# Kernel optimization log

Measured on AMD Instinct MI355X. Metric: run time of the kernel, lower is better.

## Reference

```python
import jax, jax.numpy as jnp
import numpy as np

N_NODES = 50000
N_EDGES = 800000
IN_CH, HID_CH, OUT_CH = 128, 128, 64


def setup_inputs() -> dict:
    key = jax.random.key(0)
    k1, k2, k3, k4 = jax.random.split(key, 4)
    x = jax.random.normal(k1, (N_NODES, IN_CH), dtype=jnp.float32)
    edge_index = jax.random.randint(k2, (2, N_EDGES), 0, N_NODES, dtype=jnp.int64)
    # Glorot-style scaled weights (as in PyG GCNConv default init)
    W1 = jax.random.normal(k3, (IN_CH, HID_CH), dtype=jnp.float32) * (1.0 / np.sqrt(IN_CH))
    b1 = jnp.zeros((HID_CH,), dtype=jnp.float32)
    W2 = jax.random.normal(k4, (HID_CH, OUT_CH), dtype=jnp.float32) * (1.0 / np.sqrt(HID_CH))
    b2 = jnp.zeros((OUT_CH,), dtype=jnp.float32)
    return {"x": x, "edge_index": edge_index, "W1": W1, "b1": b1, "W2": W2, "b2": b2}


def _gcn_conv(x, src, dst, norm, W, b, n_nodes):
    # linear transform, then normalized gather-scatter aggregation
    h = x @ W                                   # [N, C_out]
    msgs = h[src] * norm[:, None]               # [E+N, C_out]
    agg = jax.ops.segment_sum(msgs, dst, num_segments=n_nodes)
    return agg + b


def reference(x, edge_index, W1, b1, W2, b2):
    n = x.shape[0]
    # add self-loops (PyG GCNConv default)
    loops = jnp.arange(n, dtype=edge_index.dtype)
    src = jnp.concatenate([edge_index[0], loops])  # message source (x_j)
    dst = jnp.concatenate([edge_index[1], loops])  # aggregation target
    # symmetric normalization: deg computed over targets incl. self-loops
    deg = jax.ops.segment_sum(jnp.ones_like(dst, dtype=x.dtype), dst, num_segments=n)
    dinv = jnp.where(deg > 0, jax.lax.rsqrt(deg), 0.0)
    norm = dinv[src] * dinv[dst]                # [E+N]

    h = _gcn_conv(x, src, dst, norm, W1, b1, n)
    h = jax.nn.relu(h)
    out = _gcn_conv(h, src, dst, norm, W2, b2, n)
    return out
```

## Files before the change

kernel.cpp:

```cpp
#include <hip/hip_runtime.h>
#include <hip/hip_bf16.h>


#define NPB 196
#define NBMAX 1024
#define CAP 4096

__device__ __forceinline__ unsigned short f2bf(float f) {
    unsigned int u = __float_as_uint(f);
    unsigned int r = u + 0x7fffu + ((u >> 16) & 1u);
    return (unsigned short)(r >> 16);
}

__global__ void k_zerob(int* __restrict__ p, int n) {
    int i = blockIdx.x * blockDim.x + threadIdx.x;
    if (i < n) p[i] = 0;
}

__global__ __launch_bounds__(256) void k_bhist(const int* __restrict__ dst,
                                               int* __restrict__ bhist,
                                               int nb, int e) {
    __shared__ int hist[NBMAX];
    const int tid = threadIdx.x;
    for (int b = tid; b < nb; b += 256) hist[b] = 0;
    __syncthreads();
    for (int i = blockIdx.x * 256 + tid; i < e; i += gridDim.x * 256)
        atomicAdd(&hist[dst[i] / NPB], 1);
    __syncthreads();
    for (int b = tid; b < nb; b += 256)
        if (hist[b]) atomicAdd(&bhist[b], hist[b]);
}

__global__ __launch_bounds__(64) void k_bscan(const int* __restrict__ bhist,
                                              int* __restrict__ bbase,
                                              int* __restrict__ bcursor,
                                              int nb, int e) {
    const int lane = threadIdx.x;
    int carry = 0;
    for (int base = 0; base < nb; base += 64) {
        int i = base + lane;
        int v = (i < nb) ? bhist[i] : 0;
        int s = v;
#pragma unroll
        for (int d = 1; d < 64; d <<= 1) {
            int u = __shfl_up(s, d);
            if (lane >= d) s += u;
        }
        int excl = carry + s - v;
        if (i < nb) { bbase[i] = excl; bcursor[i] = excl; }
        carry += __shfl(s, 63);
    }
    if (lane == 0) bbase[nb] = e;
}

__global__ __launch_bounds__(256) void k_bpart(const int* __restrict__ src,
                                               const int* __restrict__ dst,
                                               int* __restrict__ bcursor,
                                               int2* __restrict__ part,
                                               int nb, int e, int cpb) {
    __shared__ int chist[NBMAX];
    __shared__ int cbase[NBMAX];
    const int tid = threadIdx.x;
    const int e0 = blockIdx.x * cpb;
    const int e1 = min(e, e0 + cpb);
    for (int b = tid; b < nb; b += 256) chist[b] = 0;
    __syncthreads();
    for (int i = e0 + tid; i < e1; i += 256)
        atomicAdd(&chist[dst[i] / NPB], 1);
    __syncthreads();
    for (int b = tid; b < nb; b += 256) {
        int c = chist[b];
        cbase[b] = c ? atomicAdd(&bcursor[b], c) : 0;
        chist[b] = 0;
    }
    __syncthreads();
    for (int i = e0 + tid; i < e1; i += 256) {
        int d = dst[i];
        int bkt = d / NPB;
        int l = atomicAdd(&chist[bkt], 1);
        part[cbase[bkt] + l] = make_int2(src[i], d);
    }
}

__global__ __launch_bounds__(256) void k_bcsr(const int2* __restrict__ part,
                                              const int* __restrict__ bbase,
                                              int* __restrict__ offs,
                                              float* __restrict__ dinv,
                                              int* __restrict__ srcs,
                                              int n, int e) {
    __shared__ int cntL[256];
    __shared__ int srcsL[CAP];
    const int b = blockIdx.x;
    const int tid = threadIdx.x;
    const int eb0 = bbase[b], eb1 = bbase[b + 1];
    const int cnt = eb1 - eb0;
    const int n0 = b * NPB;
    const int npb = min(NPB, n - n0);

    if (tid < 256) cntL[tid] = 0;
    __syncthreads();
    for (int i = eb0 + tid; i < eb1; i += 256)
        atomicAdd(&cntL[part[i].y - n0], 1);
    __syncthreads();

    if (tid < 64) {
        const int lane = tid;
        int carry = 0;
        for (int base = 0; base < npb; base += 64) {
            int i = base + lane;
            int v = (i < npb) ? cntL[i] : 0;
            int s = v;
#pragma unroll
            for (int d = 1; d < 64; d <<= 1) {
                int u = __shfl_up(s, d);
                if (lane >= d) s += u;
            }
            int excl = carry + s - v;
            if (i < npb) {
                offs[n0 + i] = eb0 + excl;
                dinv[n0 + i] = rsqrtf((float)(v + 1));
                cntL[i] = excl;
            }
            carry += __shfl(s, 63);
        }
    }
    if (b == gridDim.x - 1 && tid == 0) offs[n] = e;
    __syncthreads();

    if (cnt <= CAP) {
        for (int i = eb0 + tid; i < eb1; i += 256) {
            int2 pr = part[i];
            int pos = atomicAdd(&cntL[pr.y - n0], 1);
            srcsL[pos] = pr.x;
        }
        __syncthreads();
        for (int i = tid; i < cnt; i += 256)
            srcs[eb0 + i] = srcsL[i];
    } else {
        for (int i = eb0 + tid; i < eb1; i += 256) {
            int2 pr = part[i];
            int pos = atomicAdd(&cntL[pr.y - n0], 1);
            srcs[eb0 + pos] = pr.x;
        }
    }
}

template <int BN, bool RELU_A>
__global__ __launch_bounds__(256) void k_gemm(const float* __restrict__ A,
                                              const float* __restrict__ W,
                                              const float* __restrict__ dinv,
                                              unsigned short* __restrict__ Cout,
                                              int M, int Ntot) {
    __shared__ float As[64][132];
    __shared__ float Bs[128][BN];

    const int tid = threadIdx.x;
    const int bm = blockIdx.x * 64;
    const int bn = blockIdx.y * BN;

    constexpr int WF4 = 128 * BN / 4;
    for (int idx = tid; idx < WF4; idx += 256) {
        int row = idx / (BN / 4);
        int c4 = idx % (BN / 4);
        float4 v = *(const float4*)&W[row * Ntot + bn + c4 * 4];
        *(float4*)&Bs[row][c4 * 4] = v;
    }
    for (int idx = tid; idx < 64 * 32; idx += 256) {
        int row = idx >> 5;
        int c4 = idx & 31;
        int gr = bm + row;
        float4 v = make_float4(0.f, 0.f, 0.f, 0.f);
        if (gr < M) v = *(const float4*)&A[gr * 128 + c4 * 4];
        if (RELU_A) {
            v.x = fmaxf(v.x, 0.f); v.y = fmaxf(v.y, 0.f);
            v.z = fmaxf(v.z, 0.f); v.w = fmaxf(v.w, 0.f);
        }
        *(float4*)&As[row][c4 * 4] = v;
    }
    __syncthreads();

    const int ty = tid >> 4;
    const int tx = tid & 15;
    float acc[4][4] = {};

    for (int k = 0; k < 128; k += 4) {
        float av[4][4], bv[4][4];
#pragma unroll
        for (int i = 0; i < 4; ++i) {
            float4 t = *(const float4*)&As[ty * 4 + i][k];
            av[i][0] = t.x; av[i][1] = t.y; av[i][2] = t.z; av[i][3] = t.w;
        }
#pragma unroll
        for (int kk = 0; kk < 4; ++kk) {
            float4 t = *(const float4*)&Bs[k + kk][tx * 4];
            bv[kk][0] = t.x; bv[kk][1] = t.y; bv[kk][2] = t.z; bv[kk][3] = t.w;
        }
#pragma unroll
        for (int i = 0; i < 4; ++i)
#pragma unroll
            for (int kk = 0; kk < 4; ++kk)
#pragma unroll
                for (int j = 0; j < 4; ++j)
                    acc[i][j] = fmaf(av[i][kk], bv[kk][j], acc[i][j]);
    }

#pragma unroll
    for (int i = 0; i < 4; ++i) {
        int gr = bm + ty * 4 + i;
        if (gr < M) {
            float s = dinv[gr];
            ushort4 o;
            o.x = f2bf(acc[i][0] * s); o.y = f2bf(acc[i][1] * s);
            o.z = f2bf(acc[i][2] * s); o.w = f2bf(acc[i][3] * s);
            *(ushort4*)&Cout[(size_t)gr * Ntot + bn + tx * 4] = o;
        }
    }
}

template <int C>
__global__ __launch_bounds__(256) void k_aggr(const unsigned short* __restrict__ hs,
                                              const int* __restrict__ srcs,
                                              const int* __restrict__ offs,
                                              const float* __restrict__ dinv,
                                              const float* __restrict__ bias,
                                              float* __restrict__ outp, int n) {
    constexpr int ROWB = C * 2;
    constexpr int LPE  = ROWB / 16;
    constexpr int EPL  = 64 / LPE;
    constexpr int CHUNK = 16;
    __shared__ __align__(1024) char smem[4][CHUNK * ROWB];

    const int lane = threadIdx.x & 63;
    const int wid  = threadIdx.x >> 6;
    const int node = blockIdx.x * 4 + wid;
    if (node >= n) return;
    char* region = smem[wid];

    float2 acc = make_float2(0.f, 0.f);

    const int off = offs[node], end = offs[node + 1];
    for (int base = off; base < end; base += 64) {
        const int m = end - base;
        int p = 0;
        if (lane < m) p = srcs[base + lane];
        const int cnt = m < 64 ? m : 64;

        for (int j0 = 0; j0 < cnt; j0 += CHUNK) {
            const int cc = min(CHUNK, cnt - j0);
            const int nload = (cc + EPL - 1) / EPL;
            for (int l = 0; l < nload; ++l) {
                int e = j0 + l * EPL + (lane / LPE);
                int srow = __shfl(p, e);
                const char* ga = (const char*)hs + (size_t)srow * ROWB + (lane % LPE) * 16;
                __builtin_amdgcn_global_load_lds(
                    (const __attribute__((address_space(1))) unsigned int*)ga,
                    (__attribute__((address_space(3))) unsigned int*)(region + l * 1024),
                    16, 0, 0);
            }
            asm volatile("s_waitcnt vmcnt(0)" ::: "memory");
            __builtin_amdgcn_sched_barrier(0);

            if (C == 128) {
                for (int j = 0; j < cc; ++j) {
                    unsigned int u = *(const unsigned int*)(region + j * ROWB + lane * 4);
                    acc.x += __uint_as_float(u << 16);
                    acc.y += __uint_as_float(u & 0xffff0000u);
                }
            } else {
                const int half = lane >> 5;
                const int rounds = (cc + 1) >> 1;
                for (int r = 0; r < rounds; ++r) {
                    int e = r * 2 + half;
                    unsigned int u = *(const unsigned int*)(region + e * ROWB + (lane & 31) * 4);
                    if (e >= cc) u = 0u;
                    acc.x += __uint_as_float(u << 16);
                    acc.y += __uint_as_float(u & 0xffff0000u);
                }
            }
        }
    }

    if (C == 128) {
        unsigned int u = *(const unsigned int*)((const char*)hs + (size_t)node * ROWB + lane * 4);
        acc.x += __uint_as_float(u << 16);
        acc.y += __uint_as_float(u & 0xffff0000u);
        float di = dinv[node];
        float2 bb = *(const float2*)&bias[lane * 2];
        acc.x = fmaf(acc.x, di, bb.x);
        acc.y = fmaf(acc.y, di, bb.y);
        *(float2*)&outp[(size_t)node * C + lane * 2] = acc;
    } else {
        acc.x += __shfl_xor(acc.x, 32);
        acc.y += __shfl_xor(acc.y, 32);
        if (lane < 32) {
            unsigned int u = *(const unsigned int*)((const char*)hs + (size_t)node * ROWB + lane * 4);
            acc.x += __uint_as_float(u << 16);
            acc.y += __uint_as_float(u & 0xffff0000u);
            float di = dinv[node];
            float2 bb = *(const float2*)&bias[lane * 2];
            acc.x = fmaf(acc.x, di, bb.x);
            acc.y = fmaf(acc.y, di, bb.y);
            *(float2*)&outp[(size_t)node * C + lane * 2] = acc;
        }
    }
}

extern "C" void kernel_launch(void* const* d_in, const int* in_sizes, int n_in,
                              void* d_out, int out_size, void* d_ws, size_t ws_size,
                              hipStream_t stream) {
    const float* x  = (const float*)d_in[0];
    const int*   ei = (const int*)d_in[1];
    const float* W1 = (const float*)d_in[2];
    const float* b1 = (const float*)d_in[3];
    const float* W2 = (const float*)d_in[4];
    const float* b2 = (const float*)d_in[5];
    float* out = (float*)d_out;

    const int N = in_sizes[0] / 128;
    const int E = in_sizes[1] / 2;
    const int* src = ei;
    const int* dst = ei + E;
    const int NB = (N + NPB - 1) / NPB;
    const int CPB = (E + 255) / 256;

    char* wsb = (char*)d_ws;
    size_t o = 0;
    auto alloc = [&](size_t bytes, size_t align) {
        o = (o + align - 1) & ~(align - 1);
        char* p = wsb + o;
        o += bytes;
        return p;
    };
    int*   bhist  = (int*)alloc((size_t)NB * 4, 4);
    int*   bbase  = (int*)alloc((size_t)(NB + 1) * 4, 4);
    int*   bcur   = (int*)alloc((size_t)NB * 4, 4);
    int2*  part   = (int2*)alloc((size_t)E * 8, 8);
    int*   offs   = (int*)alloc((size_t)(N + 1) * 4, 4);
    float* dinv   = (float*)alloc((size_t)N * 4, 4);
    int*   srcs   = (int*)alloc((size_t)E * 4, 4);
    unsigned short* hs1 = (unsigned short*)alloc((size_t)N * 128 * 2, 16);
    unsigned short* hs2 = (unsigned short*)alloc((size_t)N * 64 * 2, 16);
    float* agg1   = (float*)alloc((size_t)N * 128 * 4, 16);

    k_zerob<<<1, 1024, 0, stream>>>(bhist, NB);
    k_bhist<<<256, 256, 0, stream>>>(dst, bhist, NB, E);
    k_bscan<<<1, 64, 0, stream>>>(bhist, bbase, bcur, NB, E);
    k_bpart<<<256, 256, 0, stream>>>(src, dst, bcur, part, NB, E, CPB);
    k_bcsr<<<NB, 256, 0, stream>>>(part, bbase, offs, dinv, srcs, N, E);

    const int gm = (N + 63) / 64;
    const int ga = (N + 3) / 4;

    k_gemm<64, false><<<dim3(gm, 2), 256, 0, stream>>>(x, W1, dinv, hs1, N, 128);
    k_aggr<128><<<ga, 256, 0, stream>>>(hs1, srcs, offs, dinv, b1, agg1, N);

    k_gemm<64, true><<<dim3(gm, 1), 256, 0, stream>>>(agg1, W2, dinv, hs2, N, 64);
    k_aggr<64><<<ga, 256, 0, stream>>>(hs2, srcs, offs, dinv, b2, out, N);
}
```

Baseline: 168.5 us.

## Use bf16 MFMA for GEMMs and store layer-1 output as relu'd bf16

```diff
diff --git a/kernel.cpp b/kernel.cpp
--- a/kernel.cpp
+++ b/kernel.cpp
@@ -5,6 +5,9 @@
 #define NPB 196
 #define NBMAX 1024
 #define CAP 4096
+
+using short8 = __attribute__((ext_vector_type(8))) short;
+using f32x4  = __attribute__((ext_vector_type(4))) float;
 
 __device__ __forceinline__ unsigned short f2bf(float f) {
     unsigned int u = __float_as_uint(f);
@@ -145,85 +148,105 @@
     }
 }
 
-template <int BN, bool RELU_A>
-__global__ __launch_bounds__(256) void k_gemm(const float* __restrict__ A,
+template <bool SRC_BF16>
+__global__ __launch_bounds__(256) void k_gemm(const void* __restrict__ A,
                                               const float* __restrict__ W,
                                               const float* __restrict__ dinv,
                                               unsigned short* __restrict__ Cout,
                                               int M, int Ntot) {
-    __shared__ float As[64][132];
-    __shared__ float Bs[128][BN];
+    __shared__ __align__(16) unsigned short As_b[64][136];
+    __shared__ __align__(16) unsigned short Bs_b[64][136];
 
     const int tid = threadIdx.x;
     const int bm = blockIdx.x * 64;
-    const int bn = blockIdx.y * BN;
-
-    constexpr int WF4 = 128 * BN / 4;
-    for (int idx = tid; idx < WF4; idx += 256) {
-        int row = idx / (BN / 4);
-        int c4 = idx % (BN / 4);
-        float4 v = *(const float4*)&W[row * Ntot + bn + c4 * 4];
-        *(float4*)&Bs[row][c4 * 4] = v;
-    }
-    for (int idx = tid; idx < 64 * 32; idx += 256) {
+    const int bn = blockIdx.y * 64;
+
+#pragma unroll
+    for (int t = 0; t < 8; ++t) {
+        int idx = tid + t * 256;
         int row = idx >> 5;
         int c4 = idx & 31;
         int gr = bm + row;
-        float4 v = make_float4(0.f, 0.f, 0.f, 0.f);
-        if (gr < M) v = *(const float4*)&A[gr * 128 + c4 * 4];
-        if (RELU_A) {
-            v.x = fmaxf(v.x, 0.f); v.y = fmaxf(v.y, 0.f);
-            v.z = fmaxf(v.z, 0.f); v.w = fmaxf(v.w, 0.f);
-        }
-        *(float4*)&As[row][c4 * 4] = v;
-    }
-    __syncthreads();
-
-    const int ty = tid >> 4;
-    const int tx = tid & 15;
-    float acc[4][4] = {};
-
-    for (int k = 0; k < 128; k += 4) {
-        float av[4][4], bv[4][4];
-#pragma unroll
-        for (int i = 0; i < 4; ++i) {
-            float4 t = *(const float4*)&As[ty * 4 + i][k];
-            av[i][0] = t.x; av[i][1] = t.y; av[i][2] = t.z; av[i][3] = t.w;
-        }
-#pragma unroll
-        for (int kk = 0; kk < 4; ++kk) {
-            float4 t = *(const float4*)&Bs[k + kk][tx * 4];
-            bv[kk][0] = t.x; bv[kk][1] = t.y; bv[kk][2] = t.z; bv[kk][3] = t.w;
-        }
-#pragma unroll
-        for (int i = 0; i < 4; ++i)
-#pragma unroll
-            for (int kk = 0; kk < 4; ++kk)
-#pragma unroll
-                for (int j = 0; j < 4; ++j)
-                    acc[i][j] = fmaf(av[i][kk], bv[kk][j], acc[i][j]);
-    }
-
-#pragma unroll
-    for (int i = 0; i < 4; ++i) {
-        int gr = bm + ty * 4 + i;
-        if (gr < M) {
-            float s = dinv[gr];
-            ushort4 o;
-            o.x = f2bf(acc[i][0] * s); o.y = f2bf(acc[i][1] * s);
-            o.z = f2bf(acc[i][2] * s); o.w = f2bf(acc[i][3] * s);
-            *(ushort4*)&Cout[(size_t)gr * Ntot + bn + tx * 4] = o;
-        }
-    }
-}
-
-template <int C>
+        ushort4 o = make_ushort4(0, 0, 0, 0);
+        if (SRC_BF16) {
+            if (gr < M)
+                o = *(const ushort4*)&((const unsigned short*)A)[(size_t)gr * 128 + c4 * 4];
+        } else {
+            if (gr < M) {
+                float4 f = *(const float4*)&((const float*)A)[(size_t)gr * 128 + c4 * 4];
+                o = make_ushort4(f2bf(f.x), f2bf(f.y), f2bf(f.z), f2bf(f.w));
+            }
+        }
+        *(ushort4*)&As_b[row][c4 * 4] = o;
+    }
+
+#pragma unroll
+    for (int t = 0; t < 2; ++t) {
+        int idx = tid + t * 256;
+        int kb = idx >> 4;
+        int c4 = idx & 15;
+        int k0 = kb * 4;
+        float4 f0 = *(const float4*)&W[(size_t)(k0 + 0) * Ntot + bn + c4 * 4];
+        float4 f1 = *(const float4*)&W[(size_t)(k0 + 1) * Ntot + bn + c4 * 4];
+        float4 f2 = *(const float4*)&W[(size_t)(k0 + 2) * Ntot + bn + c4 * 4];
+        float4 f3 = *(const float4*)&W[(size_t)(k0 + 3) * Ntot + bn + c4 * 4];
+        *(ushort4*)&Bs_b[c4 * 4 + 0][k0] =
+            make_ushort4(f2bf(f0.x), f2bf(f1.x), f2bf(f2.x), f2bf(f3.x));
+        *(ushort4*)&Bs_b[c4 * 4 + 1][k0] =
+            make_ushort4(f2bf(f0.y), f2bf(f1.y), f2bf(f2.y), f2bf(f3.y));
+        *(ushort4*)&Bs_b[c4 * 4 + 2][k0] =
+            make_ushort4(f2bf(f0.z), f2bf(f1.z), f2bf(f2.z), f2bf(f3.z));
+        *(ushort4*)&Bs_b[c4 * 4 + 3][k0] =
+            make_ushort4(f2bf(f0.w), f2bf(f1.w), f2bf(f2.w), f2bf(f3.w));
+    }
+    __syncthreads();
+
+    const int w = tid >> 6;
+    const int l = tid & 63;
+    const int wr = (w >> 1) * 32;
+    const int wc = (w & 1) * 32;
+    const int fr = l & 15;
+    const int fk = (l >> 4) * 8;
+
+    f32x4 acc[2][2] = {};
+
+#pragma unroll
+    for (int ks = 0; ks < 4; ++ks) {
+        const int kof = ks * 32 + fk;
+        short8 a0 = *(const short8*)&As_b[wr + fr][kof];
+        short8 a1 = *(const short8*)&As_b[wr + 16 + fr][kof];
+        short8 b0 = *(const short8*)&Bs_b[wc + fr][kof];
+        short8 b1 = *(const short8*)&Bs_b[wc + 16 + fr][kof];
+        acc[0][0] = __builtin_amdgcn_mfma_f32_16x16x32_bf16(a0, b0, acc[0][0], 0, 0, 0);
+        acc[0][1] = __builtin_amdgcn_mfma_f32_16x16x32_bf16(a0, b1, acc[0][1], 0, 0, 0);
+        acc[1][0] = __builtin_amdgcn_mfma_f32_16x16x32_bf16(a1, b0, acc[1][0], 0, 0, 0);
+        acc[1][1] = __builtin_amdgcn_mfma_f32_16x16x32_bf16(a1, b1, acc[1][1], 0, 0, 0);
+    }
+
+#pragma unroll
+    for (int i = 0; i < 2; ++i) {
+#pragma unroll
+        for (int r = 0; r < 4; ++r) {
+            int gr = bm + wr + i * 16 + ((l >> 4) << 2) + r;
+            if (gr < M) {
+                float s = dinv[gr];
+#pragma unroll
+                for (int j = 0; j < 2; ++j) {
+                    int gc = bn + wc + j * 16 + (l & 15);
+                    Cout[(size_t)gr * Ntot + gc] = f2bf(acc[i][j][r] * s);
+                }
+            }
+        }
+    }
+}
+
+template <int C, bool OBF>
 __global__ __launch_bounds__(256) void k_aggr(const unsigned short* __restrict__ hs,
                                               const int* __restrict__ srcs,
                                               const int* __restrict__ offs,
                                               const float* __restrict__ dinv,
                                               const float* __restrict__ bias,
-                                              float* __restrict__ outp, int n) {
+                                              void* __restrict__ outp, int n) {
     constexpr int ROWB = C * 2;
     constexpr int LPE  = ROWB / 16;
     constexpr int EPL  = 64 / LPE;
@@ -280,27 +303,25 @@
         }
     }
 
-    if (C == 128) {
+    if (C == 64) {
+        acc.x += __shfl_xor(acc.x, 32);
+        acc.y += __shfl_xor(acc.y, 32);
+        if (lane >= 32) return;
+    }
+    {
         unsigned int u = *(const unsigned int*)((const char*)hs + (size_t)node * ROWB + lane * 4);
         acc.x += __uint_as_float(u << 16);
         acc.y += __uint_as_float(u & 0xffff0000u);
         float di = dinv[node];
         float2 bb = *(const float2*)&bias[lane * 2];
-        acc.x = fmaf(acc.x, di, bb.x);
-        acc.y = fmaf(acc.y, di, bb.y);
-        *(float2*)&outp[(size_t)node * C + lane * 2] = acc;
-    } else {
-        acc.x += __shfl_xor(acc.x, 32);
-        acc.y += __shfl_xor(acc.y, 32);
-        if (lane < 32) {
-            unsigned int u = *(const unsigned int*)((const char*)hs + (size_t)node * ROWB + lane * 4);
-            acc.x += __uint_as_float(u << 16);
-            acc.y += __uint_as_float(u & 0xffff0000u);
-            float di = dinv[node];
-            float2 bb = *(const float2*)&bias[lane * 2];
-            acc.x = fmaf(acc.x, di, bb.x);
-            acc.y = fmaf(acc.y, di, bb.y);
-            *(float2*)&outp[(size_t)node * C + lane * 2] = acc;
+        float vx = fmaf(acc.x, di, bb.x);
+        float vy = fmaf(acc.y, di, bb.y);
+        if (OBF) {
+            unsigned short* ob = (unsigned short*)outp;
+            ushort2 o = make_ushort2(f2bf(fmaxf(vx, 0.f)), f2bf(fmaxf(vy, 0.f)));
+            *(ushort2*)&ob[(size_t)node * C + lane * 2] = o;
+        } else {
+            *(float2*)&((float*)outp)[(size_t)node * C + lane * 2] = make_float2(vx, vy);
         }
     }
 }
@@ -338,9 +359,9 @@
     int*   offs   = (int*)alloc((size_t)(N + 1) * 4, 4);
     float* dinv   = (float*)alloc((size_t)N * 4, 4);
     int*   srcs   = (int*)alloc((size_t)E * 4, 4);
-    unsigned short* hs1 = (unsigned short*)alloc((size_t)N * 128 * 2, 16);
-    unsigned short* hs2 = (unsigned short*)alloc((size_t)N * 64 * 2, 16);
-    float* agg1   = (float*)alloc((size_t)N * 128 * 4, 16);
+    unsigned short* hs1   = (unsigned short*)alloc((size_t)N * 128 * 2, 16);
+    unsigned short* hs2   = (unsigned short*)alloc((size_t)N * 64 * 2, 16);
+    unsigned short* agg1b = (unsigned short*)alloc((size_t)N * 128 * 2, 16);
 
     k_zerob<<<1, 1024, 0, stream>>>(bhist, NB);
     k_bhist<<<256, 256, 0, stream>>>(dst, bhist, NB, E);
@@ -351,9 +372,9 @@
     const int gm = (N + 63) / 64;
     const int ga = (N + 3) / 4;
 
-    k_gemm<64, false><<<dim3(gm, 2), 256, 0, stream>>>(x, W1, dinv, hs1, N, 128);
-    k_aggr<128><<<ga, 256, 0, stream>>>(hs1, srcs, offs, dinv, b1, agg1, N);
-
-    k_gemm<64, true><<<dim3(gm, 1), 256, 0, stream>>>(agg1, W2, dinv, hs2, N, 64);
-    k_aggr<64><<<ga, 256, 0, stream>>>(hs2, srcs, offs, dinv, b2, out, N);
-}
+    k_gemm<false><<<dim3(gm, 2), 256, 0, stream>>>(x, W1, dinv, hs1, N, 128);
+    k_aggr<128, true><<<ga, 256, 0, stream>>>(hs1, srcs, offs, dinv, b1, agg1b, N);
+
+    k_gemm<true><<<dim3(gm, 1), 256, 0, stream>>>(agg1b, W2, dinv, hs2, N, 64);
+    k_aggr<64, false><<<ga, 256, 0, stream>>>(hs2, srcs, offs, dinv, b2, out, N);
+}
```

After: 136.3 us, median of 2. 1.24x faster.
